# Performance work log

Measured on AMD Instinct MI355X. Metric: run time of the kernel, lower is better.

## Reference

```python
import jax, jax.numpy as jnp
import numpy as np

N_NODES = 100000
N_EDGES = 1600000
IN_DIM = 4
HID = 64


def gcn_conv(x, src, dst, W, b, num_nodes):
    """PyG GCNConv: out = D^-1/2 (A+I) D^-1/2 (x @ W) + b, add aggregation."""
    loop = jnp.arange(num_nodes)
    src_f = jnp.concatenate([src, loop])  # [E+N]
    dst_f = jnp.concatenate([dst, loop])
    # degree from destination (col) counts, self loops included -> deg >= 1
    deg = jax.ops.segment_sum(jnp.ones_like(dst_f, dtype=x.dtype), dst_f,
                              num_segments=num_nodes)
    dinv = jax.lax.rsqrt(deg)
    norm = dinv[src_f] * dinv[dst_f]  # [E+N]
    h = x @ W  # [N, out] transform first (cheaper when out <= in is false too; matches PyG)
    msg = h[src_f] * norm[:, None]  # [E+N, out]
    out = jax.ops.segment_sum(msg, dst_f, num_segments=num_nodes)
    return out + b


def setup_inputs() -> dict:
    key = jax.random.key(0)
    ks = jax.random.split(key, 6)
    x = jax.random.normal(ks[0], (N_NODES, IN_DIM), dtype=jnp.float32)
    edge_index = jax.random.randint(ks[1], (2, N_EDGES), 0, N_NODES, dtype=jnp.int64)
    # glorot-ish scaled weights
    W1 = jax.random.normal(ks[2], (IN_DIM, HID), dtype=jnp.float32) / np.sqrt(IN_DIM)
    b1 = jnp.zeros((HID,), dtype=jnp.float32)
    W2 = jax.random.normal(ks[3], (HID, HID), dtype=jnp.float32) / np.sqrt(HID)
    b2 = jnp.zeros((HID,), dtype=jnp.float32)
    Wl = jax.random.normal(ks[4], (HID, 1), dtype=jnp.float32) / np.sqrt(HID)
    bl = jnp.zeros((1,), dtype=jnp.float32)
    return {"x": x, "edge_index": edge_index, "W1": W1, "b1": b1,
            "W2": W2, "b2": b2, "Wl": Wl, "bl": bl}


def reference(x, edge_index, W1, b1, W2, b2, Wl, bl):
    num_nodes = x.shape[0]
    src, dst = edge_index[0], edge_index[1]
    h = jax.nn.relu(gcn_conv(x, src, dst, W1, b1, num_nodes))
    h = jax.nn.relu(gcn_conv(h, src, dst, W2, b2, num_nodes))
    logits = (h @ Wl + bl).squeeze(-1)  # [N]
    return logits
```

## Files before the change

kernel.cpp:

```cpp
#include <hip/hip_runtime.h>

#define NN 100000
#define NE 1600000
#define HID 64
#define NBUK 391
#define SRCBITS 17
#define SRCMASK 0x1FFFF
#define EBLK 4096
#define GE2 ((NE + EBLK - 1) / EBLK)
#define BSTRIDE 6144

typedef __attribute__((ext_vector_type(8))) short bf16x8;
typedef __attribute__((ext_vector_type(4))) float f32x4;

__device__ __forceinline__ unsigned short f2bf(float f) {
    unsigned int x = __float_as_uint(f);
    return (unsigned short)((x + 0x7FFFu + ((x >> 16) & 1u)) >> 16);
}
__device__ __forceinline__ float bflo(unsigned int u) { return __uint_as_float(u << 16); }
__device__ __forceinline__ float bfhi(unsigned int u) { return __uint_as_float(u & 0xFFFF0000u); }

__global__ void __launch_bounds__(256)
k_fill1(const int* __restrict__ ei, int* __restrict__ gcnt,
        int* __restrict__ arrival, int* __restrict__ bucketBase,
        unsigned int* __restrict__ bbuf) {
    __shared__ int s_src[EBLK];
    __shared__ int s_dst[EBLK];
    __shared__ int s_hist[NBUK];
    __shared__ int s_tmp[256];
    __shared__ int s_flag;
    __shared__ int s_last;
    int t = threadIdx.x;
    int b = blockIdx.x;

    for (int i = t; i < NBUK; i += 256) s_hist[i] = 0;
    if (t < 64) {
        unsigned long long bal = __ballot(ei[2 * t + 1] != 0);
        if (t == 0) s_flag = (bal == 0ULL) ? 1 : 0;
    }
    __syncthreads();
    int f = s_flag;
    int base = b * EBLK;
    int m = NE - base; if (m > EBLK) m = EBLK;

    if (f) {
        const int4* ps = (const int4*)ei;
        const int4* pd = (const int4*)(ei + 2 * (size_t)NE);
#pragma unroll
        for (int k = 0; k < EBLK / 512; ++k) {
            int e = base + k * 512 + t * 2;
            if (e < NE) {
                int4 vs = ps[e >> 1];
                int4 vd = pd[e >> 1];
                int l = e - base;
                s_src[l] = vs.x;     s_dst[l] = vd.x;
                s_src[l + 1] = vs.z; s_dst[l + 1] = vd.z;
                atomicAdd(&s_hist[vd.x >> 8], 1);
                atomicAdd(&s_hist[vd.z >> 8], 1);
            }
        }
    } else {
        const int4* ps = (const int4*)ei;
        const int4* pd = (const int4*)(ei + NE);
#pragma unroll
        for (int k = 0; k < EBLK / 1024; ++k) {
            int e = base + k * 1024 + t * 4;
            if (e < NE) {
                int4 vs = ps[e >> 2];
                int4 vd = pd[e >> 2];
                int l = e - base;
                s_src[l] = vs.x; s_src[l + 1] = vs.y; s_src[l + 2] = vs.z; s_src[l + 3] = vs.w;
                s_dst[l] = vd.x; s_dst[l + 1] = vd.y; s_dst[l + 2] = vd.z; s_dst[l + 3] = vd.w;
                atomicAdd(&s_hist[vd.x >> 8], 1);
                atomicAdd(&s_hist[vd.y >> 8], 1);
                atomicAdd(&s_hist[vd.z >> 8], 1);
                atomicAdd(&s_hist[vd.w >> 8], 1);
            }
        }
    }
    __syncthreads();
    for (int i = t; i < NBUK; i += 256) {
        int c = s_hist[i];
        int r = atomicAdd(&gcnt[i], c);
        s_hist[i] = i * BSTRIDE + r;
    }
    __syncthreads();
    for (int e = t; e < m; e += 256) {
        int d = s_dst[e];
        int p = atomicAdd(&s_hist[d >> 8], 1);
        bbuf[p] = ((unsigned int)(d & 255) << SRCBITS) | (unsigned int)s_src[e];
    }
    __syncthreads();
    if (t == 0) s_last = atomicAdd(arrival, 1);
    __syncthreads();
    if (s_last == GE2 - 1) {
        int i0 = 2 * t, i1 = 2 * t + 1;
        int v0 = (i0 < NBUK) ? atomicAdd(&gcnt[i0], 0) : 0;
        int v1 = (i1 < NBUK) ? atomicAdd(&gcnt[i1], 0) : 0;
        int ps2 = v0 + v1;
        s_tmp[t] = ps2; __syncthreads();
        for (int off = 1; off < 256; off <<= 1) {
            int u = (t >= off) ? s_tmp[t - off] : 0;
            __syncthreads();
            s_tmp[t] += u;
            __syncthreads();
        }
        int run = s_tmp[t] - ps2;
        if (i0 <= NBUK) bucketBase[i0] = run;
        if (i1 <= NBUK) bucketBase[i1] = run + v0;
    }
}

__global__ void k_passB(const unsigned int* __restrict__ bbuf, const int* __restrict__ gcnt,
                        const int* __restrict__ bucketBase, const float* __restrict__ x,
                        int* __restrict__ cnt, int* __restrict__ offs,
                        float* __restrict__ dinv, float* __restrict__ xs,
                        int* __restrict__ csr) {
    __shared__ int hist[256];
    __shared__ int scn[256];
    __shared__ int cur[256];
    int t = threadIdx.x;
    int b = blockIdx.x;
    int sz = gcnt[b];
    int csrbase = bucketBase[b];
    const unsigned int* buf = bbuf + (size_t)b * BSTRIDE;
    hist[t] = 0;
    __syncthreads();
    for (int e = t; e < sz; e += 256)
        atomicAdd(&hist[buf[e] >> SRCBITS], 1);
    __syncthreads();
    int deg = hist[t];
    scn[t] = deg; __syncthreads();
    for (int off = 1; off < 256; off <<= 1) {
        int u = (t >= off) ? scn[t - off] : 0;
        __syncthreads();
        scn[t] += u;
        __syncthreads();
    }
    int myoff = csrbase + scn[t] - deg;
    int node = b * 256 + t;
    if (node < NN) {
        cnt[node]  = deg;
        offs[node] = myoff;
        float d = 1.0f / sqrtf((float)(deg + 1));
        dinv[node] = d;
        float4 xv = ((const float4*)x)[node];
        float4 o; o.x = d * xv.x; o.y = d * xv.y; o.z = d * xv.z; o.w = d * xv.w;
        ((float4*)xs)[node] = o;
    }
    cur[t] = myoff;
    __syncthreads();
    for (int e = t; e < sz; e += 256) {
        unsigned int u = buf[e];
        int p = atomicAdd(&cur[u >> SRCBITS], 1);
        csr[p] = (int)(u & SRCMASK);
    }
}

__global__ void k_mm2(const float* __restrict__ xs, const int* __restrict__ cnt,
                      const int* __restrict__ offs, const int* __restrict__ csr,
                      const float* __restrict__ dinv,
                      const float* __restrict__ W1, const float* __restrict__ b1,
                      const float* __restrict__ W2, unsigned short* __restrict__ hs) {
    __shared__ unsigned short h1b[64 * 72];
    __shared__ unsigned short w2t[64 * 72];
    __shared__ float4 sPart[256];
    __shared__ float4 sAgg[64];
    __shared__ float4 sXs[64];
    __shared__ float sW1[256];
    __shared__ float sb1[64];
    __shared__ float sdv[64];
    __shared__ int scnt[64];
    __shared__ int soff[64];
    int t = threadIdx.x;
    int base = blockIdx.x * 64;
    if (t < 64) {
        int g = base + t;
        bool ok = (g < NN);
        scnt[t] = ok ? cnt[g] : 0;
        soff[t] = ok ? offs[g] : 0;
        sdv[t]  = ok ? dinv[g] : 0.f;
        sXs[t]  = ok ? ((const float4*)xs)[g] : make_float4(0.f, 0.f, 0.f, 0.f);
        sb1[t]  = b1[t];
    }
    sW1[t] = W1[t];
    for (int i = t; i < 4096; i += 256) {
        int k = i >> 6, n = i & 63;
        w2t[n * 72 + k] = f2bf(W2[i]);
    }
    if (blockIdx.x == 0 && t >= 128 && t < 192) hs[NN * 64 + (t - 128)] = 0;
    __syncthreads();
    {
        int node_l = t & 63, part = t >> 6;
        int n = scnt[node_l], b0 = soff[node_l];
        float4 s = make_float4(0.f, 0.f, 0.f, 0.f);
        int j = part;
        for (; j + 4 < n; j += 8) {
            int s0 = csr[b0 + j], s1 = csr[b0 + j + 4];
            float4 v0 = ((const float4*)xs)[s0];
            float4 v1 = ((const float4*)xs)[s1];
            s.x += v0.x + v1.x; s.y += v0.y + v1.y;
            s.z += v0.z + v1.z; s.w += v0.w + v1.w;
        }
        for (; j < n; j += 4) {
            int s0 = csr[b0 + j];
            float4 v = ((const float4*)xs)[s0];
            s.x += v.x; s.y += v.y; s.z += v.z; s.w += v.w;
        }
        sPart[t] = s;
    }
    __syncthreads();
    if (t < 64) {
        float4 a = sPart[t], b = sPart[t + 64], c = sPart[t + 128], d = sPart[t + 192];
        float4 xi = sXs[t];
        float dn = sdv[t];
        float4 o;
        o.x = dn * (a.x + b.x + c.x + d.x + xi.x);
        o.y = dn * (a.y + b.y + c.y + d.y + xi.y);
        o.z = dn * (a.z + b.z + c.z + d.z + xi.z);
        o.w = dn * (a.w + b.w + c.w + d.w + xi.w);
        sAgg[t] = o;
    }
    __syncthreads();
#pragma unroll
    for (int i = 0; i < 16; ++i) {
        int e = i * 256 + t;
        int nl = e >> 6, c = e & 63;
        float4 a = sAgg[nl];
        float h = fmaf(a.x, sW1[c], fmaf(a.y, sW1[64 + c],
                  fmaf(a.z, sW1[128 + c], fmaf(a.w, sW1[192 + c], sb1[c]))));
        h1b[nl * 72 + c] = f2bf(fmaxf(h, 0.f));
    }
    __syncthreads();
    int w = t >> 6, lane = t & 63, l15 = lane & 15, quad = lane >> 4;
    bf16x8 a0 = *(const bf16x8*)&h1b[(w * 16 + l15) * 72 + quad * 8];
    bf16x8 a1 = *(const bf16x8*)&h1b[(w * 16 + l15) * 72 + 32 + quad * 8];
    f32x4 acc[4];
#pragma unroll
    for (int nt = 0; nt < 4; ++nt) {
        bf16x8 bb0 = *(const bf16x8*)&w2t[(nt * 16 + l15) * 72 + quad * 8];
        bf16x8 bb1 = *(const bf16x8*)&w2t[(nt * 16 + l15) * 72 + 32 + quad * 8];
        f32x4 c = {0.f, 0.f, 0.f, 0.f};
        c = __builtin_amdgcn_mfma_f32_16x16x32_bf16(a0, bb0, c, 0, 0, 0);
        c = __builtin_amdgcn_mfma_f32_16x16x32_bf16(a1, bb1, c, 0, 0, 0);
        acc[nt] = c;
    }
#pragma unroll
    for (int nt = 0; nt < 4; ++nt) {
#pragma unroll
        for (int r = 0; r < 4; ++r) {
            int localn = w * 16 + quad * 4 + r;
            int g = base + localn;
            if (g < NN) hs[g * 64 + nt * 16 + l15] = f2bf(acc[nt][r] * sdv[localn]);
        }
    }
}

__global__ void k_gather_head(const unsigned short* __restrict__ hs, const int* __restrict__ offs,
                              const int* __restrict__ cnt, const int* __restrict__ csr,
                              const float* __restrict__ dinv, const float* __restrict__ b2,
                              const float* __restrict__ Wl, const float* __restrict__ bl,
                              float* __restrict__ out) {
    int t = threadIdx.x;
    int c = t & 63;
    int g = c >> 4;
    int sl = c & 15;
    int node = blockIdx.x * 16 + (t >> 6) * 4 + g;
    int b = offs[node], n = cnt[node];
    const uint2* hrow = (const uint2*)hs;
    const int* ce = csr + b;
    float4 A = make_float4(0.f, 0.f, 0.f, 0.f);
#define ACC2(u) do { \
    A.x += bflo(u.x); A.y += bfhi(u.x); A.z += bflo(u.y); A.w += bfhi(u.y); } while (0)
    for (int j = 0; j < n; j += 4) {
        int i0 = ce[j];
        int i1 = (j + 1 < n) ? ce[j + 1] : NN;
        int i2 = (j + 2 < n) ? ce[j + 2] : NN;
        int i3 = (j + 3 < n) ? ce[j + 3] : NN;
        uint2 u0 = hrow[i0 * 16 + sl];
        uint2 u1 = hrow[i1 * 16 + sl];
        uint2 u2 = hrow[i2 * 16 + sl];
        uint2 u3 = hrow[i3 * 16 + sl];
        ACC2(u0); ACC2(u1); ACC2(u2); ACC2(u3);
    }
    uint2 uS = hrow[node * 16 + sl];
    ACC2(uS);
#undef ACC2
    float4 bv = ((const float4*)b2)[sl];
    float4 wv = ((const float4*)Wl)[sl];
    float dn = dinv[node];
    float v = fmaxf(fmaf(dn, A.x, bv.x), 0.f) * wv.x
            + fmaxf(fmaf(dn, A.y, bv.y), 0.f) * wv.y
            + fmaxf(fmaf(dn, A.z, bv.z), 0.f) * wv.z
            + fmaxf(fmaf(dn, A.w, bv.w), 0.f) * wv.w;
    v += __shfl_xor(v, 1, 64);
    v += __shfl_xor(v, 2, 64);
    v += __shfl_xor(v, 4, 64);
    v += __shfl_xor(v, 8, 64);
    if (sl == 0) out[node] = v + bl[0];
}

extern "C" void kernel_launch(void* const* d_in, const int* in_sizes, int n_in,
                              void* d_out, int out_size, void* d_ws, size_t ws_size,
                              hipStream_t stream) {
    const float* x  = (const float*)d_in[0];
    const int*   ei = (const int*)d_in[1];
    const float* W1 = (const float*)d_in[2];
    const float* b1 = (const float*)d_in[3];
    const float* W2 = (const float*)d_in[4];
    const float* b2 = (const float*)d_in[5];
    const float* Wl = (const float*)d_in[6];
    const float* bl = (const float*)d_in[7];
    float* out = (float*)d_out;

    char* w = (char*)d_ws;
    float* dinv  = (float*)w;                  w += NN * 4;
    int*   cnt   = (int*)w;                    w += NN * 4;
    int*   offs  = (int*)w;                    w += NN * 4;
    int*   csr   = (int*)w;                    w += NE * 4;
    float* xs    = (float*)w;                  w += NN * 4 * 4;
    unsigned short* hs = (unsigned short*)w;   w += (size_t)(NN + 1) * HID * 2;
    int*   gcnt  = (int*)w;                    w += NBUK * 4;
    int*   arrival = (int*)w;                  w += 4;
    int*   bucketBase = (int*)w;               w += (NBUK + 1) * 4;
    w = (char*)(((size_t)w + 255) & ~(size_t)255);
    unsigned int* bbuf = (unsigned int*)w;     w += (size_t)NBUK * BSTRIDE * 4;

    const int GMM = (NN + 63) / 64;

    hipMemsetAsync(gcnt, 0, (NBUK + 1) * sizeof(int), stream);
    hipLaunchKernelGGL(k_fill1, dim3(GE2),  dim3(256), 0, stream,
                       ei, gcnt, arrival, bucketBase, bbuf);
    hipLaunchKernelGGL(k_passB, dim3(NBUK), dim3(256), 0, stream,
                       bbuf, gcnt, bucketBase, x, cnt, offs, dinv, xs, csr);
    hipLaunchKernelGGL(k_mm2, dim3(GMM), dim3(256), 0, stream,
                       xs, cnt, offs, csr, dinv, W1, b1, W2, hs);
    hipLaunchKernelGGL(k_gather_head, dim3(NN / 16), dim3(256), 0, stream,
                       hs, offs, cnt, csr, dinv, b2, Wl, bl, out);
}
```

Baseline: 172.1 us.

## Pad CSR rows to multiples of four with sentinel and use fixed per-bucket strides

Drops the last-block global prefix scan over bucket counts by giving each bucket a fixed CSR stride. Pads each node's neighbor list to a multiple of four with a sentinel index pointing at a zero row, so both gather kernels read indices as int4 with no tail handling. k_passB stages the bucket buffer in shared memory instead of reading it from global twice. This costs extra CSR padding memory and writes, and assumes no bucket exceeds the stride.

```diff
diff --git a/kernel.cpp b/kernel.cpp
--- a/kernel.cpp
+++ b/kernel.cpp
@@ -9,6 +9,7 @@
 #define EBLK 4096
 #define GE2 ((NE + EBLK - 1) / EBLK)
 #define BSTRIDE 6144
+#define CSTRIDE 6144
 
 typedef __attribute__((ext_vector_type(8))) short bf16x8;
 typedef __attribute__((ext_vector_type(4))) float f32x4;
@@ -22,14 +23,11 @@
 
 __global__ void __launch_bounds__(256)
 k_fill1(const int* __restrict__ ei, int* __restrict__ gcnt,
-        int* __restrict__ arrival, int* __restrict__ bucketBase,
         unsigned int* __restrict__ bbuf) {
     __shared__ int s_src[EBLK];
     __shared__ int s_dst[EBLK];
     __shared__ int s_hist[NBUK];
-    __shared__ int s_tmp[256];
     __shared__ int s_flag;
-    __shared__ int s_last;
     int t = threadIdx.x;
     int b = blockIdx.x;
 
@@ -81,7 +79,7 @@
     __syncthreads();
     for (int i = t; i < NBUK; i += 256) {
         int c = s_hist[i];
-        int r = atomicAdd(&gcnt[i], c);
+        int r = c ? atomicAdd(&gcnt[i], c) : 0;
         s_hist[i] = i * BSTRIDE + r;
     }
     __syncthreads();
@@ -90,54 +88,38 @@
         int p = atomicAdd(&s_hist[d >> 8], 1);
         bbuf[p] = ((unsigned int)(d & 255) << SRCBITS) | (unsigned int)s_src[e];
     }
-    __syncthreads();
-    if (t == 0) s_last = atomicAdd(arrival, 1);
-    __syncthreads();
-    if (s_last == GE2 - 1) {
-        int i0 = 2 * t, i1 = 2 * t + 1;
-        int v0 = (i0 < NBUK) ? atomicAdd(&gcnt[i0], 0) : 0;
-        int v1 = (i1 < NBUK) ? atomicAdd(&gcnt[i1], 0) : 0;
-        int ps2 = v0 + v1;
-        s_tmp[t] = ps2; __syncthreads();
-        for (int off = 1; off < 256; off <<= 1) {
-            int u = (t >= off) ? s_tmp[t - off] : 0;
-            __syncthreads();
-            s_tmp[t] += u;
-            __syncthreads();
-        }
-        int run = s_tmp[t] - ps2;
-        if (i0 <= NBUK) bucketBase[i0] = run;
-        if (i1 <= NBUK) bucketBase[i1] = run + v0;
-    }
-}
-
-__global__ void k_passB(const unsigned int* __restrict__ bbuf, const int* __restrict__ gcnt,
-                        const int* __restrict__ bucketBase, const float* __restrict__ x,
-                        int* __restrict__ cnt, int* __restrict__ offs,
-                        float* __restrict__ dinv, float* __restrict__ xs,
-                        int* __restrict__ csr) {
+}
+
+__global__ void __launch_bounds__(256)
+k_passB(const unsigned int* __restrict__ bbuf, const int* __restrict__ gcnt,
+        const float* __restrict__ x, int* __restrict__ cnt, int* __restrict__ offs,
+        float* __restrict__ dinv, float* __restrict__ xs, int* __restrict__ csr) {
+    __shared__ unsigned int s_buf[BSTRIDE];
     __shared__ int hist[256];
     __shared__ int scn[256];
     __shared__ int cur[256];
     int t = threadIdx.x;
     int b = blockIdx.x;
     int sz = gcnt[b];
-    int csrbase = bucketBase[b];
     const unsigned int* buf = bbuf + (size_t)b * BSTRIDE;
     hist[t] = 0;
     __syncthreads();
-    for (int e = t; e < sz; e += 256)
-        atomicAdd(&hist[buf[e] >> SRCBITS], 1);
+    for (int e = t; e < sz; e += 256) {
+        unsigned int u = buf[e];
+        s_buf[e] = u;
+        atomicAdd(&hist[u >> SRCBITS], 1);
+    }
     __syncthreads();
     int deg = hist[t];
-    scn[t] = deg; __syncthreads();
+    int pdeg = (deg + 3) & ~3;
+    scn[t] = pdeg; __syncthreads();
     for (int off = 1; off < 256; off <<= 1) {
         int u = (t >= off) ? scn[t - off] : 0;
         __syncthreads();
         scn[t] += u;
         __syncthreads();
     }
-    int myoff = csrbase + scn[t] - deg;
+    int myoff = b * CSTRIDE + scn[t] - pdeg;
     int node = b * 256 + t;
     if (node < NN) {
         cnt[node]  = deg;
@@ -148,13 +130,16 @@
         float4 o; o.x = d * xv.x; o.y = d * xv.y; o.z = d * xv.z; o.w = d * xv.w;
         ((float4*)xs)[node] = o;
     }
+    for (int p = deg; p < pdeg; ++p) csr[myoff + p] = NN;
     cur[t] = myoff;
     __syncthreads();
     for (int e = t; e < sz; e += 256) {
-        unsigned int u = buf[e];
+        unsigned int u = s_buf[e];
         int p = atomicAdd(&cur[u >> SRCBITS], 1);
         csr[p] = (int)(u & SRCMASK);
     }
+    if (b == 0 && t == 0)
+        ((float4*)xs)[NN] = make_float4(0.f, 0.f, 0.f, 0.f);
 }
 
 __global__ void k_mm2(const float* __restrict__ xs, const int* __restrict__ cnt,
@@ -192,20 +177,20 @@
     __syncthreads();
     {
         int node_l = t & 63, part = t >> 6;
-        int n = scnt[node_l], b0 = soff[node_l];
+        int n = scnt[node_l];
+        const int4* cp4 = (const int4*)csr;
+        int nb = soff[node_l] >> 2;
         float4 s = make_float4(0.f, 0.f, 0.f, 0.f);
-        int j = part;
-        for (; j + 4 < n; j += 8) {
-            int s0 = csr[b0 + j], s1 = csr[b0 + j + 4];
-            float4 v0 = ((const float4*)xs)[s0];
-            float4 v1 = ((const float4*)xs)[s1];
-            s.x += v0.x + v1.x; s.y += v0.y + v1.y;
-            s.z += v0.z + v1.z; s.w += v0.w + v1.w;
-        }
-        for (; j < n; j += 4) {
-            int s0 = csr[b0 + j];
-            float4 v = ((const float4*)xs)[s0];
-            s.x += v.x; s.y += v.y; s.z += v.z; s.w += v.w;
+        for (int c = part; c * 4 < n; c += 4) {
+            int4 q = cp4[nb + c];
+            float4 v0 = ((const float4*)xs)[q.x];
+            float4 v1 = ((const float4*)xs)[q.y];
+            float4 v2 = ((const float4*)xs)[q.z];
+            float4 v3 = ((const float4*)xs)[q.w];
+            s.x += (v0.x + v1.x) + (v2.x + v3.x);
+            s.y += (v0.y + v1.y) + (v2.y + v3.y);
+            s.z += (v0.z + v1.z) + (v2.z + v3.z);
+            s.w += (v0.w + v1.w) + (v2.w + v3.w);
         }
         sPart[t] = s;
     }
@@ -266,21 +251,19 @@
     int g = c >> 4;
     int sl = c & 15;
     int node = blockIdx.x * 16 + (t >> 6) * 4 + g;
-    int b = offs[node], n = cnt[node];
+    int n = cnt[node];
     const uint2* hrow = (const uint2*)hs;
-    const int* ce = csr + b;
+    const int4* cp4 = (const int4*)csr;
+    int nb = offs[node] >> 2;
     float4 A = make_float4(0.f, 0.f, 0.f, 0.f);
 #define ACC2(u) do { \
     A.x += bflo(u.x); A.y += bfhi(u.x); A.z += bflo(u.y); A.w += bfhi(u.y); } while (0)
-    for (int j = 0; j < n; j += 4) {
-        int i0 = ce[j];
-        int i1 = (j + 1 < n) ? ce[j + 1] : NN;
-        int i2 = (j + 2 < n) ? ce[j + 2] : NN;
-        int i3 = (j + 3 < n) ? ce[j + 3] : NN;
-        uint2 u0 = hrow[i0 * 16 + sl];
-        uint2 u1 = hrow[i1 * 16 + sl];
-        uint2 u2 = hrow[i2 * 16 + sl];
-        uint2 u3 = hrow[i3 * 16 + sl];
+    for (int j4 = 0; j4 * 4 < n; ++j4) {
+        int4 q = cp4[nb + j4];
+        uint2 u0 = hrow[q.x * 16 + sl];
+        uint2 u1 = hrow[q.y * 16 + sl];
+        uint2 u2 = hrow[q.z * 16 + sl];
+        uint2 u3 = hrow[q.w * 16 + sl];
         ACC2(u0); ACC2(u1); ACC2(u2); ACC2(u3);
     }
     uint2 uS = hrow[node * 16 + sl];
@@ -317,23 +300,18 @@
     float* dinv  = (float*)w;                  w += NN * 4;
     int*   cnt   = (int*)w;                    w += NN * 4;
     int*   offs  = (int*)w;                    w += NN * 4;
-    int*   csr   = (int*)w;                    w += NE * 4;
-    float* xs    = (float*)w;                  w += NN * 4 * 4;
+    float* xs    = (float*)w;                  w += (size_t)(NN + 1) * 16;
     unsigned short* hs = (unsigned short*)w;   w += (size_t)(NN + 1) * HID * 2;
-    int*   gcnt  = (int*)w;                    w += NBUK * 4;
-    int*   arrival = (int*)w;                  w += 4;
-    int*   bucketBase = (int*)w;               w += (NBUK + 1) * 4;
+    int*   gcnt  = (int*)w;                    w += ((NBUK + 3) & ~3) * 4;
+    int*   csr   = (int*)w;                    w += (size_t)NBUK * CSTRIDE * 4;
     w = (char*)(((size_t)w + 255) & ~(size_t)255);
     unsigned int* bbuf = (unsigned int*)w;     w += (size_t)NBUK * BSTRIDE * 4;
 
-    const int GMM = (NN + 63) / 64;
-
-    hipMemsetAsync(gcnt, 0, (NBUK + 1) * sizeof(int), stream);
-    hipLaunchKernelGGL(k_fill1, dim3(GE2),  dim3(256), 0, stream,
-                       ei, gcnt, arrival, bucketBase, bbuf);
+    hipMemsetAsync(gcnt, 0, NBUK * sizeof(int), stream);
+    hipLaunchKernelGGL(k_fill1, dim3(GE2),  dim3(256), 0, stream, ei, gcnt, bbuf);
     hipLaunchKernelGGL(k_passB, dim3(NBUK), dim3(256), 0, stream,
-                       bbuf, gcnt, bucketBase, x, cnt, offs, dinv, xs, csr);
-    hipLaunchKernelGGL(k_mm2, dim3(GMM), dim3(256), 0, stream,
+                       bbuf, gcnt, x, cnt, offs, dinv, xs, csr);
+    hipLaunchKernelGGL(k_mm2, dim3((NN + 63) / 64), dim3(256), 0, stream,
                        xs, cnt, offs, csr, dinv, W1, b1, W2, hs);
     hipLaunchKernelGGL(k_gather_head, dim3(NN / 16), dim3(256), 0, stream,
                        hs, offs, cnt, csr, dinv, b2, Wl, bl, out);
```

Result: slower. 182.0 us (+5.8%).
